# Optimization experiments

Hardware: AMD Instinct MI355X
Metric: run time of the kernel (lower is better)

The kernel has to match this reference:

```python
import jax, jax.numpy as jnp
import numpy as np

N_NODES = 100000
IN_DIM, H_DIM, OUT_DIM = 256, 128, 40
N_EDGES = 1600000


def gcn_conv(x, edge_index, W, b, n_nodes):
    # PyG GCNConv: add self-loops, symmetric norm D^-1/2 A D^-1/2, linear, aggregate, + bias
    loop = jnp.arange(n_nodes, dtype=edge_index.dtype)
    src = jnp.concatenate([edge_index[0], loop])
    dst = jnp.concatenate([edge_index[1], loop])
    deg = jax.ops.segment_sum(jnp.ones_like(dst, dtype=x.dtype), dst, num_segments=n_nodes)
    dinv = jax.lax.rsqrt(jnp.maximum(deg, 1e-12))
    norm = dinv[src] * dinv[dst]                      # [E+N]
    h = x @ W                                         # [N, out]
    msg = h[src] * norm[:, None]                      # [E+N, out]
    out = jax.ops.segment_sum(msg, dst, num_segments=n_nodes)
    return out + b


def setup_inputs() -> dict:
    key = jax.random.key(0)
    k1, k2, k3, k4, k5, k6 = jax.random.split(key, 6)
    x = jax.random.normal(k1, (N_NODES, IN_DIM), dtype=jnp.float32)
    edge_index = jax.random.randint(k2, (2, N_EDGES), 0, N_NODES, dtype=jnp.int64)
    s1 = 1.0 / np.sqrt(IN_DIM)
    s2 = 1.0 / np.sqrt(H_DIM)
    W1 = jax.random.uniform(k3, (IN_DIM, H_DIM), jnp.float32, -s1, s1)
    b1 = jax.random.uniform(k4, (H_DIM,), jnp.float32, -s1, s1)
    W2 = jax.random.uniform(k5, (H_DIM, OUT_DIM), jnp.float32, -s2, s2)
    b2 = jax.random.uniform(k6, (OUT_DIM,), jnp.float32, -s2, s2)
    return {"x": x, "edge_index": edge_index, "W1": W1, "b1": b1, "W2": W2, "b2": b2}


def reference(x, edge_index, W1, b1, W2, b2):
    n = x.shape[0]
    h = gcn_conv(x, edge_index, W1, b1, n)
    h = jax.nn.relu(h)  # dropout is identity at eval
    out = gcn_conv(h, edge_index, W2, b2, n)
    return out
```

## Files before the change

kernel.cpp:

```cpp
#include <hip/hip_runtime.h>

#define NODES 100000
#define INDIM 256
#define HDIM 128
#define ODIM 40
#define NPX 12500

typedef short bf16x8 __attribute__((ext_vector_type(8)));
typedef float f32x16 __attribute__((ext_vector_type(16)));


__global__ __launch_bounds__(256) void k_hist(const int* __restrict__ dst, int E,
                                              int* __restrict__ counts){
    int xcd = blockIdx.x & 7;
    int g   = blockIdx.x >> 3;
    int lo = xcd * NPX, hi = lo + NPX;
    for(int e = g * 256 + threadIdx.x; e < E; e += 65536){
        int d = dst[e];
        if(d >= lo && d < hi) atomicAdd(&counts[d], 1);
    }
}

__global__ __launch_bounds__(256) void k_fill(const int* __restrict__ src, const int* __restrict__ dst,
                                              int E, int* __restrict__ cursor, int* __restrict__ esrc){
    int xcd = blockIdx.x & 7;
    int g   = blockIdx.x >> 3;
    int lo = xcd * NPX, hi = lo + NPX;
    for(int e = g * 256 + threadIdx.x; e < E; e += 65536){
        int d = dst[e];
        if(d >= lo && d < hi){
            int p = atomicAdd(&cursor[d], 1);
            esrc[p] = src[e];
        }
    }
}

__global__ void k_psum(const int* __restrict__ counts, int* __restrict__ partial, int n){
    __shared__ int sm[256];
    int chunk = (n + 255) >> 8;
    int start = blockIdx.x * chunk;
    int end = min(start + chunk, n);
    int s = 0;
    for(int i = start + threadIdx.x; i < end; i += 256) s += counts[i];
    sm[threadIdx.x] = s;
    __syncthreads();
    for(int off = 128; off > 0; off >>= 1){
        if(threadIdx.x < off) sm[threadIdx.x] += sm[threadIdx.x + off];
        __syncthreads();
    }
    if(threadIdx.x == 0) partial[blockIdx.x] = sm[0];
}

__global__ void k_scan256(const int* __restrict__ partial, int* __restrict__ pscan){
    __shared__ int sm[256];
    int t = threadIdx.x;
    sm[t] = partial[t];
    __syncthreads();
    for(int off = 1; off < 256; off <<= 1){
        int v = (t >= off) ? sm[t - off] : 0;
        __syncthreads();
        sm[t] += v;
        __syncthreads();
    }
    pscan[t] = (t == 0) ? 0 : sm[t - 1];
}

__global__ void k_scan_final(const int* __restrict__ counts, const int* __restrict__ pscan,
                             int n, int E, int* __restrict__ row_start, int* __restrict__ cursor,
                             float* __restrict__ dinv){
    __shared__ int sm[512];
    int chunk = (n + 255) >> 8;
    int b = blockIdx.x, t = threadIdx.x;
    int idx = b * chunk + t;
    int c = (t < chunk && idx < n) ? counts[idx] : 0;
    sm[t] = c;
    __syncthreads();
    for(int off = 1; off < 512; off <<= 1){
        int v = (t >= off) ? sm[t - off] : 0;
        __syncthreads();
        sm[t] += v;
        __syncthreads();
    }
    if(t < chunk && idx < n){
        int rs = pscan[b] + sm[t] - c;
        row_start[idx] = rs;
        cursor[idx] = rs;
        dinv[idx] = rsqrtf((float)(c + 1));
    }
    if(b == 0 && t == 0) row_start[n] = E;
}

__global__ void k_wsplit(const float* __restrict__ W, unsigned short* __restrict__ whi,
                         unsigned short* __restrict__ wlo){
    int t = blockIdx.x * 256 + threadIdx.x;
    int lane = t & 63;
    int kk = (t >> 6) & 15;
    int cf = t >> 10;
    int col = cf * 32 + (lane & 31);
    int kbase = kk * 16 + (lane >> 5) * 8;
    #pragma unroll
    for(int i = 0; i < 8; ++i){
        float f = W[(size_t)(kbase + i) * HDIM + col];
        unsigned u = __float_as_uint(f);
        unsigned short hs = (unsigned short)(u >> 16);
        float lf = f - __uint_as_float(u & 0xffff0000u);
        unsigned short ls = (unsigned short)(__float_as_uint(lf) >> 16);
        whi[(size_t)t * 8 + i] = hs;
        wlo[(size_t)t * 8 + i] = ls;
    }
}

__device__ inline void split8(const float4 v0, const float4 v1, bf16x8& hi, bf16x8& lo){
    const float f[8] = {v0.x, v0.y, v0.z, v0.w, v1.x, v1.y, v1.z, v1.w};
    #pragma unroll
    for(int i = 0; i < 8; ++i){
        unsigned u = __float_as_uint(f[i]);
        hi[i] = (short)(u >> 16);
        float lf = f[i] - __uint_as_float(u & 0xffff0000u);
        lo[i] = (short)(__float_as_uint(lf) >> 16);
    }
}

__global__ __launch_bounds__(256, 3) void k_gemm1(const float* __restrict__ x,
        const bf16x8* __restrict__ whi, const bf16x8* __restrict__ wlo,
        const float* __restrict__ dinv, float* __restrict__ h, int n){
    int wid = blockIdx.x * 4 + (threadIdx.x >> 6);
    if(wid >= (n >> 5)) return;
    int lane = threadIdx.x & 63;
    int r  = lane & 31;
    int hk = lane >> 5;
    int row0 = wid * 32;

    f32x16 acc[4];
    #pragma unroll
    for(int cf = 0; cf < 4; ++cf)
        #pragma unroll
        for(int i = 0; i < 16; ++i) acc[cf][i] = 0.f;

    const float* ap = x + (size_t)(row0 + r) * INDIM + hk * 8;

    for(int kk = 0; kk < 16; ++kk){
        int ko = kk * 16;
        float4 a0 = *(const float4*)(ap + ko);
        float4 a1 = *(const float4*)(ap + ko + 4);
        bf16x8 bh[4], bl[4];
        #pragma unroll
        for(int cf = 0; cf < 4; ++cf){
            bh[cf] = whi[(cf * 16 + kk) * 64 + lane];
            bl[cf] = wlo[(cf * 16 + kk) * 64 + lane];
        }
        bf16x8 ah, al;
        split8(a0, a1, ah, al);
        #pragma unroll
        for(int cf = 0; cf < 4; ++cf){
            acc[cf] = __builtin_amdgcn_mfma_f32_32x32x16_bf16(ah, bh[cf], acc[cf], 0, 0, 0);
            acc[cf] = __builtin_amdgcn_mfma_f32_32x32x16_bf16(ah, bl[cf], acc[cf], 0, 0, 0);
            acc[cf] = __builtin_amdgcn_mfma_f32_32x32x16_bf16(al, bh[cf], acc[cf], 0, 0, 0);
        }
    }

    #pragma unroll
    for(int reg = 0; reg < 16; ++reg){
        int row = row0 + (reg & 3) + 8 * (reg >> 2) + 4 * hk;
        float di = dinv[row];
        float* hp = h + (size_t)row * HDIM + r;
        #pragma unroll
        for(int cf = 0; cf < 4; ++cf)
            hp[cf * 32] = acc[cf][reg] * di;
    }
}

__global__ __launch_bounds__(256) void k_gemm2(const float* __restrict__ a, const float* __restrict__ W,
                                               const float* __restrict__ dinv,
                                               float* __restrict__ h, int n){
    __shared__ float xs[64][132];
    __shared__ float ws[HDIM][ODIM];
    int tid = threadIdx.x;
    int row0 = blockIdx.x * 64;
    #pragma unroll
    for(int jj = 0; jj < 8; ++jj){
        int f = tid + 256 * jj;
        int r = f >> 5;
        int c4 = (f & 31) << 2;
        float4 v = make_float4(0.f, 0.f, 0.f, 0.f);
        int grow = row0 + r;
        if(grow < n) v = *(const float4*)&a[(size_t)grow * HDIM + c4];
        *(float4*)&xs[r][c4] = v;
    }
    #pragma unroll
    for(int jj = 0; jj < 5; ++jj){
        int f = tid + 256 * jj;
        int r = f / 10;
        int c4 = (f % 10) << 2;
        *(float4*)&ws[r][c4] = *(const float4*)&W[(size_t)r * ODIM + c4];
    }
    __syncthreads();
    int q = tid & 3, r = tid >> 2;
    float acc[10];
    #pragma unroll
    for(int j = 0; j < 10; ++j) acc[j] = 0.f;
    #pragma unroll 4
    for(int k = 0; k < HDIM; ++k){
        float xv = xs[r][k];
        #pragma unroll
        for(int j = 0; j < 5; ++j){
            float2 w = *(const float2*)&ws[k][2 * q + 8 * j];
            acc[2*j+0] += xv * w.x;
            acc[2*j+1] += xv * w.y;
        }
    }
    int grow = row0 + r;
    if(grow < n){
        float dv = dinv[grow];
        #pragma unroll
        for(int j = 0; j < 5; ++j){
            float2 o; o.x = acc[2*j] * dv; o.y = acc[2*j+1] * dv;
            *(float2*)&h[(size_t)grow * ODIM + 2 * q + 8 * j] = o;
        }
    }
}

__global__ __launch_bounds__(256) void k_agg1(const float4* __restrict__ h4, const int* __restrict__ row_start,
                                              const int* __restrict__ esrc, const float* __restrict__ dinv,
                                              const float4* __restrict__ bias4, float4* __restrict__ out4, int n){
    int wav = (blockIdx.x * 256 + threadIdx.x) >> 6;
    int lane = threadIdx.x & 63;
    int half = lane >> 5;
    int node = wav * 2 + half;
    if(node >= n) return;
    int r32 = lane & 31;

    float4 acc = h4[(size_t)node * 32 + r32];
    int e = row_start[node], e1 = row_start[node + 1];

    for(; e + 8 <= e1; e += 8){
        int s[8];
        #pragma unroll
        for(int j = 0; j < 8; ++j) s[j] = esrc[e + j];
        float4 m[8];
        #pragma unroll
        for(int j = 0; j < 8; ++j) m[j] = h4[(size_t)s[j] * 32 + r32];
        #pragma unroll
        for(int j = 0; j < 8; ++j){
            acc.x += m[j].x; acc.y += m[j].y; acc.z += m[j].z; acc.w += m[j].w;
        }
    }
    if(e + 4 <= e1){
        int s[4];
        #pragma unroll
        for(int j = 0; j < 4; ++j) s[j] = esrc[e + j];
        float4 m[4];
        #pragma unroll
        for(int j = 0; j < 4; ++j) m[j] = h4[(size_t)s[j] * 32 + r32];
        #pragma unroll
        for(int j = 0; j < 4; ++j){
            acc.x += m[j].x; acc.y += m[j].y; acc.z += m[j].z; acc.w += m[j].w;
        }
        e += 4;
    }
    for(; e < e1; ++e){
        int s = esrc[e];
        float4 m = h4[(size_t)s * 32 + r32];
        acc.x += m.x; acc.y += m.y; acc.z += m.z; acc.w += m.w;
    }

    float di = dinv[node];
    float4 b = bias4[r32];
    float4 o;
    o.x = fmaxf(fmaf(acc.x, di, b.x), 0.f);
    o.y = fmaxf(fmaf(acc.y, di, b.y), 0.f);
    o.z = fmaxf(fmaf(acc.z, di, b.z), 0.f);
    o.w = fmaxf(fmaf(acc.w, di, b.w), 0.f);
    out4[(size_t)node * 32 + r32] = o;
}

__global__ __launch_bounds__(256) void k_agg2(const float* __restrict__ h, const int* __restrict__ row_start,
                                              const int* __restrict__ esrc, const float* __restrict__ dinv,
                                              const float* __restrict__ bias, float* __restrict__ out, int n){
    int wid = (blockIdx.x * 256 + threadIdx.x) >> 6;
    int lane = threadIdx.x & 63;
    if(wid >= n || lane >= ODIM) return;
    float a = h[(size_t)wid * ODIM + lane];
    int e = row_start[wid], e1 = row_start[wid + 1];
    for(; e + 8 <= e1; e += 8){
        int s[8];
        #pragma unroll
        for(int j = 0; j < 8; ++j) s[j] = esrc[e + j];
        float m[8];
        #pragma unroll
        for(int j = 0; j < 8; ++j) m[j] = h[(size_t)s[j] * ODIM + lane];
        #pragma unroll
        for(int j = 0; j < 8; ++j) a += m[j];
    }
    if(e + 4 <= e1){
        int s[4];
        #pragma unroll
        for(int j = 0; j < 4; ++j) s[j] = esrc[e + j];
        float m[4];
        #pragma unroll
        for(int j = 0; j < 4; ++j) m[j] = h[(size_t)s[j] * ODIM + lane];
        #pragma unroll
        for(int j = 0; j < 4; ++j) a += m[j];
        e += 4;
    }
    for(; e < e1; ++e){
        int s = esrc[e];
        a += h[(size_t)s * ODIM + lane];
    }
    out[(size_t)wid * ODIM + lane] = fmaf(a, dinv[wid], bias[lane]);
}

extern "C" void kernel_launch(void* const* d_in, const int* in_sizes, int n_in,
                              void* d_out, int out_size, void* d_ws, size_t ws_size,
                              hipStream_t stream){
    const float* x  = (const float*)d_in[0];
    const int*   ei = (const int*)d_in[1];
    const float* W1 = (const float*)d_in[2];
    const float* b1 = (const float*)d_in[3];
    const float* W2 = (const float*)d_in[4];
    const float* b2 = (const float*)d_in[5];
    float* out = (float*)d_out;

    const int n = NODES;
    const int E = in_sizes[1] / 2;
    const int* esrc_in = ei;
    const int* edst_in = ei + E;

    char* w = (char*)d_ws;
    int*   counts    = (int*)(w + (0u << 19));
    int*   row_start = (int*)(w + (1u << 19));
    int*   cursor    = (int*)(w + (2u << 19));
    int*   partial   = (int*)(w + (3u << 19));
    int*   pscan     = (int*)(w + (3u << 19) + 4096);
    float* dinv      = (float*)(w + (4u << 19));
    int*   esrc      = (int*)(w + (5u << 19));
    unsigned short* whi = (unsigned short*)(w + (10u << 20));
    unsigned short* wlo = (unsigned short*)(w + (11u << 20));
    float* h1        = (float*)(w + (16u << 20));
    float* h1r       = (float*)(w + (68u << 20));
    float* h2        = h1;

    hipMemsetAsync(counts, 0, n * sizeof(int), stream);
    k_hist<<<2048, 256, 0, stream>>>(edst_in, E, counts);
    k_psum<<<256, 256, 0, stream>>>(counts, partial, n);
    k_scan256<<<1, 256, 0, stream>>>(partial, pscan);
    k_scan_final<<<256, 512, 0, stream>>>(counts, pscan, n, E, row_start, cursor, dinv);
    k_fill<<<2048, 256, 0, stream>>>(esrc_in, edst_in, E, cursor, esrc);
    k_wsplit<<<16, 256, 0, stream>>>(W1, whi, wlo);

    k_gemm1<<<(NODES / 32 + 3) / 4, 256, 0, stream>>>(x, (const bf16x8*)whi, (const bf16x8*)wlo,
                                                      dinv, h1, n);
    k_agg1<<<(n / 2 + 3) / 4, 256, 0, stream>>>((const float4*)h1, row_start, esrc, dinv,
                                                (const float4*)b1, (float4*)h1r, n);
    k_gemm2<<<(n + 63) / 64, 256, 0, stream>>>(h1r, W2, dinv, h2, n);
    k_agg2<<<(n * 64 + 255) / 256, 256, 0, stream>>>(h2, row_start, esrc, dinv, b2, out, n);
}
```

Baseline: 561.9 us.

## Pad CSR rows to multiples of eight with a zero dummy node for vectorized gathers

```diff
diff --git a/kernel.cpp b/kernel.cpp
--- a/kernel.cpp
+++ b/kernel.cpp
@@ -41,7 +41,7 @@
     int start = blockIdx.x * chunk;
     int end = min(start + chunk, n);
     int s = 0;
-    for(int i = start + threadIdx.x; i < end; i += 256) s += counts[i];
+    for(int i = start + threadIdx.x; i < end; i += 256) s += (counts[i] + 7) & ~7;
     sm[threadIdx.x] = s;
     __syncthreads();
     for(int off = 128; off > 0; off >>= 1){
@@ -66,14 +66,15 @@
 }
 
 __global__ void k_scan_final(const int* __restrict__ counts, const int* __restrict__ pscan,
-                             int n, int E, int* __restrict__ row_start, int* __restrict__ cursor,
+                             int n, int* __restrict__ row_start, int* __restrict__ cursor,
                              float* __restrict__ dinv){
     __shared__ int sm[512];
     int chunk = (n + 255) >> 8;
     int b = blockIdx.x, t = threadIdx.x;
     int idx = b * chunk + t;
     int c = (t < chunk && idx < n) ? counts[idx] : 0;
-    sm[t] = c;
+    int cp = (c + 7) & ~7;
+    sm[t] = cp;
     __syncthreads();
     for(int off = 1; off < 512; off <<= 1){
         int v = (t >= off) ? sm[t - off] : 0;
@@ -82,12 +83,20 @@
         __syncthreads();
     }
     if(t < chunk && idx < n){
-        int rs = pscan[b] + sm[t] - c;
+        int rs = pscan[b] + sm[t] - cp;
         row_start[idx] = rs;
         cursor[idx] = rs;
         dinv[idx] = rsqrtf((float)(c + 1));
-    }
-    if(b == 0 && t == 0) row_start[n] = E;
+        if(idx == n - 1) row_start[n] = rs + cp;
+    }
+}
+
+__global__ void k_pad(const int* __restrict__ cursor, const int* __restrict__ row_start,
+                      int* __restrict__ esrc, int n){
+    int i = blockIdx.x * 256 + threadIdx.x;
+    if(i >= n) return;
+    int p = cursor[i], p1 = row_start[i + 1];
+    for(; p < p1; ++p) esrc[p] = n;
 }
 
 __global__ void k_wsplit(const float* __restrict__ W, unsigned short* __restrict__ whi,
@@ -233,35 +242,51 @@
     float4 acc = h4[(size_t)node * 32 + r32];
     int e = row_start[node], e1 = row_start[node + 1];
 
-    for(; e + 8 <= e1; e += 8){
-        int s[8];
-        #pragma unroll
-        for(int j = 0; j < 8; ++j) s[j] = esrc[e + j];
-        float4 m[8];
-        #pragma unroll
-        for(int j = 0; j < 8; ++j) m[j] = h4[(size_t)s[j] * 32 + r32];
-        #pragma unroll
-        for(int j = 0; j < 8; ++j){
-            acc.x += m[j].x; acc.y += m[j].y; acc.z += m[j].z; acc.w += m[j].w;
-        }
-    }
-    if(e + 4 <= e1){
-        int s[4];
-        #pragma unroll
-        for(int j = 0; j < 4; ++j) s[j] = esrc[e + j];
-        float4 m[4];
-        #pragma unroll
-        for(int j = 0; j < 4; ++j) m[j] = h4[(size_t)s[j] * 32 + r32];
-        #pragma unroll
-        for(int j = 0; j < 4; ++j){
-            acc.x += m[j].x; acc.y += m[j].y; acc.z += m[j].z; acc.w += m[j].w;
-        }
-        e += 4;
-    }
-    for(; e < e1; ++e){
-        int s = esrc[e];
-        float4 m = h4[(size_t)s * 32 + r32];
-        acc.x += m.x; acc.y += m.y; acc.z += m.z; acc.w += m.w;
+    for(; e + 16 <= e1; e += 16){
+        int4 sa = *(const int4*)&esrc[e];
+        int4 sb = *(const int4*)&esrc[e + 4];
+        int4 sc = *(const int4*)&esrc[e + 8];
+        int4 sd = *(const int4*)&esrc[e + 12];
+        float4 m0  = h4[(size_t)sa.x * 32 + r32];
+        float4 m1  = h4[(size_t)sa.y * 32 + r32];
+        float4 m2  = h4[(size_t)sa.z * 32 + r32];
+        float4 m3  = h4[(size_t)sa.w * 32 + r32];
+        float4 m4  = h4[(size_t)sb.x * 32 + r32];
+        float4 m5  = h4[(size_t)sb.y * 32 + r32];
+        float4 m6  = h4[(size_t)sb.z * 32 + r32];
+        float4 m7  = h4[(size_t)sb.w * 32 + r32];
+        float4 m8  = h4[(size_t)sc.x * 32 + r32];
+        float4 m9  = h4[(size_t)sc.y * 32 + r32];
+        float4 m10 = h4[(size_t)sc.z * 32 + r32];
+        float4 m11 = h4[(size_t)sc.w * 32 + r32];
+        float4 m12 = h4[(size_t)sd.x * 32 + r32];
+        float4 m13 = h4[(size_t)sd.y * 32 + r32];
+        float4 m14 = h4[(size_t)sd.z * 32 + r32];
+        float4 m15 = h4[(size_t)sd.w * 32 + r32];
+        acc.x += ((m0.x + m1.x) + (m2.x + m3.x)) + ((m4.x + m5.x) + (m6.x + m7.x))
+               + ((m8.x + m9.x) + (m10.x + m11.x)) + ((m12.x + m13.x) + (m14.x + m15.x));
+        acc.y += ((m0.y + m1.y) + (m2.y + m3.y)) + ((m4.y + m5.y) + (m6.y + m7.y))
+               + ((m8.y + m9.y) + (m10.y + m11.y)) + ((m12.y + m13.y) + (m14.y + m15.y));
+        acc.z += ((m0.z + m1.z) + (m2.z + m3.z)) + ((m4.z + m5.z) + (m6.z + m7.z))
+               + ((m8.z + m9.z) + (m10.z + m11.z)) + ((m12.z + m13.z) + (m14.z + m15.z));
+        acc.w += ((m0.w + m1.w) + (m2.w + m3.w)) + ((m4.w + m5.w) + (m6.w + m7.w))
+               + ((m8.w + m9.w) + (m10.w + m11.w)) + ((m12.w + m13.w) + (m14.w + m15.w));
+    }
+    if(e < e1){
+        int4 sa = *(const int4*)&esrc[e];
+        int4 sb = *(const int4*)&esrc[e + 4];
+        float4 m0 = h4[(size_t)sa.x * 32 + r32];
+        float4 m1 = h4[(size_t)sa.y * 32 + r32];
+        float4 m2 = h4[(size_t)sa.z * 32 + r32];
+        float4 m3 = h4[(size_t)sa.w * 32 + r32];
+        float4 m4 = h4[(size_t)sb.x * 32 + r32];
+        float4 m5 = h4[(size_t)sb.y * 32 + r32];
+        float4 m6 = h4[(size_t)sb.z * 32 + r32];
+        float4 m7 = h4[(size_t)sb.w * 32 + r32];
+        acc.x += ((m0.x + m1.x) + (m2.x + m3.x)) + ((m4.x + m5.x) + (m6.x + m7.x));
+        acc.y += ((m0.y + m1.y) + (m2.y + m3.y)) + ((m4.y + m5.y) + (m6.y + m7.y));
+        acc.z += ((m0.z + m1.z) + (m2.z + m3.z)) + ((m4.z + m5.z) + (m6.z + m7.z));
+        acc.w += ((m0.w + m1.w) + (m2.w + m3.w)) + ((m4.w + m5.w) + (m6.w + m7.w));
     }
 
     float di = dinv[node];
@@ -282,30 +307,18 @@
     if(wid >= n || lane >= ODIM) return;
     float a = h[(size_t)wid * ODIM + lane];
     int e = row_start[wid], e1 = row_start[wid + 1];
-    for(; e + 8 <= e1; e += 8){
-        int s[8];
-        #pragma unroll
-        for(int j = 0; j < 8; ++j) s[j] = esrc[e + j];
-        float m[8];
-        #pragma unroll
-        for(int j = 0; j < 8; ++j) m[j] = h[(size_t)s[j] * ODIM + lane];
-        #pragma unroll
-        for(int j = 0; j < 8; ++j) a += m[j];
-    }
-    if(e + 4 <= e1){
-        int s[4];
-        #pragma unroll
-        for(int j = 0; j < 4; ++j) s[j] = esrc[e + j];
-        float m[4];
-        #pragma unroll
-        for(int j = 0; j < 4; ++j) m[j] = h[(size_t)s[j] * ODIM + lane];
-        #pragma unroll
-        for(int j = 0; j < 4; ++j) a += m[j];
-        e += 4;
-    }
-    for(; e < e1; ++e){
-        int s = esrc[e];
-        a += h[(size_t)s * ODIM + lane];
+    for(; e < e1; e += 8){
+        int4 sa = *(const int4*)&esrc[e];
+        int4 sb = *(const int4*)&esrc[e + 4];
+        float m0 = h[(size_t)sa.x * ODIM + lane];
+        float m1 = h[(size_t)sa.y * ODIM + lane];
+        float m2 = h[(size_t)sa.z * ODIM + lane];
+        float m3 = h[(size_t)sa.w * ODIM + lane];
+        float m4 = h[(size_t)sb.x * ODIM + lane];
+        float m5 = h[(size_t)sb.y * ODIM + lane];
+        float m6 = h[(size_t)sb.z * ODIM + lane];
+        float m7 = h[(size_t)sb.w * ODIM + lane];
+        a += ((m0 + m1) + (m2 + m3)) + ((m4 + m5) + (m6 + m7));
     }
     out[(size_t)wid * ODIM + lane] = fmaf(a, dinv[wid], bias[lane]);
 }
@@ -327,15 +340,15 @@
     const int* edst_in = ei + E;
 
     char* w = (char*)d_ws;
-    int*   counts    = (int*)(w + (0u << 19));
+    int*   counts    = (int*)(w);
     int*   row_start = (int*)(w + (1u << 19));
     int*   cursor    = (int*)(w + (2u << 19));
     int*   partial   = (int*)(w + (3u << 19));
     int*   pscan     = (int*)(w + (3u << 19) + 4096);
     float* dinv      = (float*)(w + (4u << 19));
-    int*   esrc      = (int*)(w + (5u << 19));
-    unsigned short* whi = (unsigned short*)(w + (10u << 20));
-    unsigned short* wlo = (unsigned short*)(w + (11u << 20));
+    unsigned short* whi = (unsigned short*)(w + (6u << 19));
+    unsigned short* wlo = (unsigned short*)(w + (7u << 19));
+    int*   esrc      = (int*)(w + (4u << 20));
     float* h1        = (float*)(w + (16u << 20));
     float* h1r       = (float*)(w + (68u << 20));
     float* h2        = h1;
@@ -344,14 +357,17 @@
     k_hist<<<2048, 256, 0, stream>>>(edst_in, E, counts);
     k_psum<<<256, 256, 0, stream>>>(counts, partial, n);
     k_scan256<<<1, 256, 0, stream>>>(partial, pscan);
-    k_scan_final<<<256, 512, 0, stream>>>(counts, pscan, n, E, row_start, cursor, dinv);
+    k_scan_final<<<256, 512, 0, stream>>>(counts, pscan, n, row_start, cursor, dinv);
     k_fill<<<2048, 256, 0, stream>>>(esrc_in, edst_in, E, cursor, esrc);
+    k_pad<<<(n + 255) / 256, 256, 0, stream>>>(cursor, row_start, esrc, n);
     k_wsplit<<<16, 256, 0, stream>>>(W1, whi, wlo);
 
     k_gemm1<<<(NODES / 32 + 3) / 4, 256, 0, stream>>>(x, (const bf16x8*)whi, (const bf16x8*)wlo,
                                                       dinv, h1, n);
+    hipMemsetAsync(h1 + (size_t)n * HDIM, 0, HDIM * sizeof(float), stream);
     k_agg1<<<(n / 2 + 3) / 4, 256, 0, stream>>>((const float4*)h1, row_start, esrc, dinv,
                                                 (const float4*)b1, (float4*)h1r, n);
     k_gemm2<<<(n + 63) / 64, 256, 0, stream>>>(h1r, W2, dinv, h2, n);
+    hipMemsetAsync(h2 + (size_t)n * ODIM, 0, ODIM * sizeof(float), stream);
     k_agg2<<<(n * 64 + 255) / 256, 256, 0, stream>>>(h2, row_start, esrc, dinv, b2, out, n);
 }
```

Measured after the change: 563.9 us. No clear change (+0.4%).
